# Optimization experiments

Measured on AMD Instinct MI355X. Metric: run time of the kernel, lower is better.

Reference implementation:

```python
import jax, jax.numpy as jnp
import numpy as np

LMDA = 1.0
SMOOTH = 1e-05

# 13 directional offsets (dz, dy, dx) matching the original slice pairs 1..13
OFFSETS = [
    (1, 0, 0), (0, 1, 0), (0, 0, 1),
    (1, 1, 0), (1, -1, 0),
    (0, 1, 1), (0, 1, -1),
    (1, 0, -1), (1, 0, 1),
    (1, -1, -1), (1, 1, -1),
    (-1, -1, -1), (-1, 1, -1),
]


def _shifted_diff(x, off):
    """x[..., pos-shift] - x[..., neg-shift] for offset off over last 3 dims."""
    sl_pos = tuple(slice(1, None) if o == 1 else (slice(None, -1) if o == -1 else slice(None)) for o in off)
    sl_neg = tuple(slice(None, -1) if o == 1 else (slice(1, None) if o == -1 else slice(None)) for o in off)
    return x[(Ellipsis,) + sl_pos] - x[(Ellipsis,) + sl_neg]


def setup_inputs() -> dict:
    key = jax.random.key(0)
    k1, k2 = jax.random.split(key)
    shape = (4, 1, 128, 192, 192)
    eps = 1e-6
    inp = jax.random.uniform(k1, shape, dtype=jnp.float32, minval=eps, maxval=1.0 - eps)
    tgt = jax.random.uniform(k2, shape, dtype=jnp.float32, minval=0.0, maxval=1.0)
    return {"input": inp, "target": tgt}


def reference(input, target):
    # region term: BCE with mean reduction
    bce = -jnp.mean(target * jnp.log(input) + (1.0 - target) * jnp.log(1.0 - input))

    # boundary term: 13 directional diff-product ratios
    acc = jnp.float32(0.0)
    for off in OFFSETS:
        di = _shifted_diff(input, off)
        dt = _shifted_diff(target, off)
        acc = acc + jnp.sum(di * dt) / (jnp.sum(dt * dt) + SMOOTH)
    boundary = 1.0 - acc / 13.0

    return LMDA * bce + boundary
```

## Files before the change

### kernel.cpp

```cpp
#include <hip/hip_runtime.h>
#include <math.h>

#define DX 192
#define DY 192
#define DZ 128
#define DB 4
#define DXY (DX*DY)
#define NTOT (DB*DZ*DXY)
#define XV (DX/4)
#define NCOL (DB*DZ*XV)
#define SEG 12
#define NSEG (DY/SEG)


__device__ inline float wred(float v) {
    #pragma unroll
    for (int o = 32; o > 0; o >>= 1) v += __shfl_down(v, o, 64);
    return v;
}

__device__ inline float4 ld4(const float* p) { return *(const float4*)p; }

#define TN(k, A1, A0, D1, D0) do { float di_=(A1)-(A0); float dt_=(D1)-(D0); \
    sk[k] += di_*dt_; rk[k] += dt_*dt_; } while(0)
#define TM(k, A1, A0, D1, D0) do { float di_=(A1)-(A0); float dt_=(D1)-(D0); \
    float dm_=fx3*dt_; sk[k] += di_*dm_; rk[k] += dt_*dm_; } while(0)
#define BCEACC(A0, D0) do { bces += (D0)*__logf(A0) + (1.0f-(D0))*__logf(1.0f-(A0)); } while(0)


#define ELEM_FULL(a0,a1,a2,a3,a4,a5,a6,a7, d0,d1,d2,d3,d4,d5,d6,d7) do { \
    TN(0,a4,a0,d4,d0); TN(1,a2,a0,d2,d0); TN(2,a1,a0,d1,d0); TN(3,a6,a0,d6,d0); \
    TN(4,a4,a2,d4,d2); TN(5,a3,a0,d3,d0); TN(6,a2,a1,d2,d1); TN(7,a4,a1,d4,d1); \
    TN(8,a5,a0,d5,d0); TN(9,a4,a3,d4,d3); TN(10,a6,a1,d6,d1); TN(11,a7,a0,d7,d0); \
    TN(12,a5,a2,d5,d2); BCEACC(a0,d0); } while(0)

#define ELEM_FX(a0,a1,a2,a3,a4,a5,a6,a7, d0,d1,d2,d3,d4,d5,d6,d7) do { \
    TN(0,a4,a0,d4,d0); TN(1,a2,a0,d2,d0); TM(2,a1,a0,d1,d0); TN(3,a6,a0,d6,d0); \
    TN(4,a4,a2,d4,d2); TM(5,a3,a0,d3,d0); TM(6,a2,a1,d2,d1); TM(7,a4,a1,d4,d1); \
    TM(8,a5,a0,d5,d0); TM(9,a4,a3,d4,d3); TM(10,a6,a1,d6,d1); TM(11,a7,a0,d7,d0); \
    TM(12,a5,a2,d5,d2); BCEACC(a0,d0); } while(0)

#define PEL_FULL(a0,a1,a4,a5, d0,d1,d4,d5) do { \
    TN(0,a4,a0,d4,d0); TN(2,a1,a0,d1,d0); TN(7,a4,a1,d4,d1); TN(8,a5,a0,d5,d0); \
    BCEACC(a0,d0); } while(0)
#define PEL_FX(a0,a1,a4,a5, d0,d1,d4,d5) do { \
    TN(0,a4,a0,d4,d0); TM(2,a1,a0,d1,d0); TM(7,a4,a1,d4,d1); TM(8,a5,a0,d5,d0); \
    BCEACC(a0,d0); } while(0)

#define ZEL_FULL(a0,a1,a2,a3, d0,d1,d2,d3) do { \
    TN(1,a2,a0,d2,d0); TN(2,a1,a0,d1,d0); TN(5,a3,a0,d3,d0); TN(6,a2,a1,d2,d1); \
    BCEACC(a0,d0); } while(0)
#define ZEL_FX(a0,a1,a2,a3, d0,d1,d2,d3) do { \
    TN(1,a2,a0,d2,d0); TM(2,a1,a0,d1,d0); TM(5,a3,a0,d3,d0); TM(6,a2,a1,d2,d1); \
    BCEACC(a0,d0); } while(0)

#define ZPEL_FULL(a0,a1, d0,d1) do { TN(2,a1,a0,d1,d0); BCEACC(a0,d0); } while(0)
#define ZPEL_FX(a0,a1, d0,d1)   do { TM(2,a1,a0,d1,d0); BCEACC(a0,d0); } while(0)

#define ROW_FULL(Ai0,Ai1,Aie, At0,At1,Ate, Bi0,Bi1,Bie, Bt0,Bt1,Bte) do { \
    ELEM_FULL(Ai0.x,Ai0.y, Bi0.x,Bi0.y, Ai1.x,Ai1.y, Bi1.x,Bi1.y, \
              At0.x,At0.y, Bt0.x,Bt0.y, At1.x,At1.y, Bt1.x,Bt1.y); \
    ELEM_FULL(Ai0.y,Ai0.z, Bi0.y,Bi0.z, Ai1.y,Ai1.z, Bi1.y,Bi1.z, \
              At0.y,At0.z, Bt0.y,Bt0.z, At1.y,At1.z, Bt1.y,Bt1.z); \
    ELEM_FULL(Ai0.z,Ai0.w, Bi0.z,Bi0.w, Ai1.z,Ai1.w, Bi1.z,Bi1.w, \
              At0.z,At0.w, Bt0.z,Bt0.w, At1.z,At1.w, Bt1.z,Bt1.w); \
    ELEM_FX  (Ai0.w,Aie,   Bi0.w,Bie,   Ai1.w,Ai1##e_, Bi1.w,Bi1##e_, \
              At0.w,Ate,   Bt0.w,Bte,   At1.w,At1##e_, Bt1.w,Bt1##e_); \
    } while(0)

__global__ __launch_bounds__(256) void gc3d_main(const float* __restrict__ inp,
                                                 const float* __restrict__ tgt,
                                                 double* __restrict__ acc) {
    float sk[13] = {0,0,0,0,0,0,0,0,0,0,0,0,0};
    float rk[13] = {0,0,0,0,0,0,0,0,0,0,0,0,0};
    float bces = 0.f;

    int c   = blockIdx.x * 256 + threadIdx.x;
    int s   = blockIdx.y;
    int xv4 = c % XV;
    int zb  = c / XV;
    int z   = zb & (DZ - 1);
    int y0  = s * SEG;
    bool xlast = (xv4 == XV - 1);
    int   xe   = xlast ? 3 : 4;
    float fx3  = xlast ? 0.f : 1.f;
    bool lastseg = (s == NSEG - 1);
    int  nfull   = SEG - (lastseg ? 1 : 0);

    int base = (zb * DY + y0) * DX + xv4 * 4;
    const float* ip = inp + base;
    const float* tp = tgt + base;

    if (z != DZ - 1) {
        float4 i0 = ld4(ip),        i1 = ld4(ip + DXY);
        float4 t0 = ld4(tp),        t1 = ld4(tp + DXY);
        float  i0e = ip[xe],        i1e = ip[DXY + xe];
        float  t0e = tp[xe],        t1e = tp[DXY + xe];
        float4 j0 = ld4(ip + DX),   j1 = ld4(ip + DX + DXY);
        float4 u0 = ld4(tp + DX),   u1 = ld4(tp + DX + DXY);
        float  j0e = ip[DX + xe],   j1e = ip[DX + DXY + xe];
        float  u0e = tp[DX + xe],   u1e = tp[DX + DXY + xe];

        #pragma unroll 2
        for (int it = 0; it < nfull - 1; ++it) {
            const float* ipk = ip + 2 * DX;
            const float* tpk = tp + 2 * DX;
            float4 k0 = ld4(ipk),       k1 = ld4(ipk + DXY);
            float4 w0 = ld4(tpk),       w1 = ld4(tpk + DXY);
            float  k0e = ipk[xe],       k1e = ipk[DXY + xe];
            float  w0e = tpk[xe],       w1e = tpk[DXY + xe];

            ELEM_FULL(i0.x,i0.y, j0.x,j0.y, i1.x,i1.y, j1.x,j1.y,
                      t0.x,t0.y, u0.x,u0.y, t1.x,t1.y, u1.x,u1.y);
            ELEM_FULL(i0.y,i0.z, j0.y,j0.z, i1.y,i1.z, j1.y,j1.z,
                      t0.y,t0.z, u0.y,u0.z, t1.y,t1.z, u1.y,u1.z);
            ELEM_FULL(i0.z,i0.w, j0.z,j0.w, i1.z,i1.w, j1.z,j1.w,
                      t0.z,t0.w, u0.z,u0.w, t1.z,t1.w, u1.z,u1.w);
            ELEM_FX  (i0.w,i0e,  j0.w,j0e,  i1.w,i1e,  j1.w,j1e,
                      t0.w,t0e,  u0.w,u0e,  t1.w,t1e,  u1.w,u1e);

            i0 = j0; i1 = j1; t0 = u0; t1 = u1;
            i0e = j0e; i1e = j1e; t0e = u0e; t1e = u1e;
            j0 = k0; j1 = k1; u0 = w0; u1 = w1;
            j0e = k0e; j1e = k1e; u0e = w0e; u1e = w1e;
            ip += DX; tp += DX;
        }
        ELEM_FULL(i0.x,i0.y, j0.x,j0.y, i1.x,i1.y, j1.x,j1.y,
                  t0.x,t0.y, u0.x,u0.y, t1.x,t1.y, u1.x,u1.y);
        ELEM_FULL(i0.y,i0.z, j0.y,j0.z, i1.y,i1.z, j1.y,j1.z,
                  t0.y,t0.z, u0.y,u0.z, t1.y,t1.z, u1.y,u1.z);
        ELEM_FULL(i0.z,i0.w, j0.z,j0.w, i1.z,i1.w, j1.z,j1.w,
                  t0.z,t0.w, u0.z,u0.w, t1.z,t1.w, u1.z,u1.w);
        ELEM_FX  (i0.w,i0e,  j0.w,j0e,  i1.w,i1e,  j1.w,j1e,
                  t0.w,t0e,  u0.w,u0e,  t1.w,t1e,  u1.w,u1e);

        if (lastseg) {
            PEL_FULL(j0.x,j0.y, j1.x,j1.y, u0.x,u0.y, u1.x,u1.y);
            PEL_FULL(j0.y,j0.z, j1.y,j1.z, u0.y,u0.z, u1.y,u1.z);
            PEL_FULL(j0.z,j0.w, j1.z,j1.w, u0.z,u0.w, u1.z,u1.w);
            PEL_FX  (j0.w,j0e,  j1.w,j1e,  u0.w,u0e,  u1.w,u1e);
        }
    } else {
        float4 i0 = ld4(ip);
        float4 t0 = ld4(tp);
        float  i0e = ip[xe];
        float  t0e = tp[xe];
        float4 j0 = ld4(ip + DX);
        float4 u0 = ld4(tp + DX);
        float  j0e = ip[DX + xe];
        float  u0e = tp[DX + xe];

        #pragma unroll 2
        for (int it = 0; it < nfull - 1; ++it) {
            const float* ipk = ip + 2 * DX;
            const float* tpk = tp + 2 * DX;
            float4 k0 = ld4(ipk);
            float4 w0 = ld4(tpk);
            float  k0e = ipk[xe];
            float  w0e = tpk[xe];

            ZEL_FULL(i0.x,i0.y, j0.x,j0.y, t0.x,t0.y, u0.x,u0.y);
            ZEL_FULL(i0.y,i0.z, j0.y,j0.z, t0.y,t0.z, u0.y,u0.z);
            ZEL_FULL(i0.z,i0.w, j0.z,j0.w, t0.z,t0.w, u0.z,u0.w);
            ZEL_FX  (i0.w,i0e,  j0.w,j0e,  t0.w,t0e,  u0.w,u0e);

            i0 = j0; t0 = u0; i0e = j0e; t0e = u0e;
            j0 = k0; u0 = w0; j0e = k0e; u0e = w0e;
            ip += DX; tp += DX;
        }
        ZEL_FULL(i0.x,i0.y, j0.x,j0.y, t0.x,t0.y, u0.x,u0.y);
        ZEL_FULL(i0.y,i0.z, j0.y,j0.z, t0.y,t0.z, u0.y,u0.z);
        ZEL_FULL(i0.z,i0.w, j0.z,j0.w, t0.z,t0.w, u0.z,u0.w);
        ZEL_FX  (i0.w,i0e,  j0.w,j0e,  t0.w,t0e,  u0.w,u0e);

        if (lastseg) {
            ZPEL_FULL(j0.x,j0.y, u0.x,u0.y);
            ZPEL_FULL(j0.y,j0.z, u0.y,u0.z);
            ZPEL_FULL(j0.z,j0.w, u0.z,u0.w);
            ZPEL_FX  (j0.w,j0e,  u0.w,u0e);
        }
    }

    float vals[27];
    #pragma unroll
    for (int q = 0; q < 13; q++) { vals[q] = sk[q]; vals[13 + q] = rk[q]; }
    vals[26] = bces;
    #pragma unroll
    for (int q = 0; q < 27; q++) vals[q] = wred(vals[q]);

    __shared__ float red[4][27];
    int lane = threadIdx.x & 63;
    int wave = threadIdx.x >> 6;
    if (lane == 0) {
        #pragma unroll
        for (int q = 0; q < 27; q++) red[wave][q] = vals[q];
    }
    __syncthreads();
    if (threadIdx.x < 27) {
        float t = red[0][threadIdx.x] + red[1][threadIdx.x]
                + red[2][threadIdx.x] + red[3][threadIdx.x];
        atomicAdd(&acc[threadIdx.x], (double)t);
    }
}

__global__ void gc3d_final(const double* __restrict__ acc, float* __restrict__ out) {
    if (threadIdx.x == 0 && blockIdx.x == 0) {
        double s = 0.0;
        #pragma unroll
        for (int k = 0; k < 13; k++) s += acc[k] / (acc[13 + k] + 1e-5);
        double bce = -acc[26] / (double)NTOT;
        out[0] = (float)(bce + 1.0 - s / 13.0);
    }
}

extern "C" void kernel_launch(void* const* d_in, const int* in_sizes, int n_in,
                              void* d_out, int out_size, void* d_ws, size_t ws_size,
                              hipStream_t stream) {
    const float* inp = (const float*)d_in[0];
    const float* tgt = (const float*)d_in[1];
    double* acc = (double*)d_ws;

    hipMemsetAsync(d_ws, 0, 27 * sizeof(double), stream);
    dim3 grid(NCOL / 256, NSEG);
    gc3d_main<<<grid, 256, 0, stream>>>(inp, tgt, acc);
    gc3d_final<<<1, 64, 0, stream>>>(acc, (float*)d_out);
}
```

Baseline: 214.5 us.

## Fully unroll row loop with deeper prefetch, smaller segments, occupancy bound

Shrinks the y-segment per thread from 12 to 8 rows, giving more blocks. The main (non-last-z) path becomes a fully unrolled sequence that loads up to three rows ahead before computing each row pair, which keeps more loads in flight. It also adds a min-blocks-per-CU launch bound of 3 to cap register use. The cost is more redundant halo-row loads per output row and more register pressure from the named row sets, which the launch bound may answer with spills.

```diff
diff --git a/kernel.cpp b/kernel.cpp
--- a/kernel.cpp
+++ b/kernel.cpp
@@ -9,7 +9,7 @@
 #define NTOT (DB*DZ*DXY)
 #define XV (DX/4)
 #define NCOL (DB*DZ*XV)
-#define SEG 12
+#define SEG 8
 #define NSEG (DY/SEG)
 
 
@@ -57,20 +57,36 @@
 #define ZPEL_FULL(a0,a1, d0,d1) do { TN(2,a1,a0,d1,d0); BCEACC(a0,d0); } while(0)
 #define ZPEL_FX(a0,a1, d0,d1)   do { TM(2,a1,a0,d1,d0); BCEACC(a0,d0); } while(0)
 
-#define ROW_FULL(Ai0,Ai1,Aie, At0,At1,Ate, Bi0,Bi1,Bie, Bt0,Bt1,Bte) do { \
-    ELEM_FULL(Ai0.x,Ai0.y, Bi0.x,Bi0.y, Ai1.x,Ai1.y, Bi1.x,Bi1.y, \
-              At0.x,At0.y, Bt0.x,Bt0.y, At1.x,At1.y, Bt1.x,Bt1.y); \
-    ELEM_FULL(Ai0.y,Ai0.z, Bi0.y,Bi0.z, Ai1.y,Ai1.z, Bi1.y,Bi1.z, \
-              At0.y,At0.z, Bt0.y,Bt0.z, At1.y,At1.z, Bt1.y,Bt1.z); \
-    ELEM_FULL(Ai0.z,Ai0.w, Bi0.z,Bi0.w, Ai1.z,Ai1.w, Bi1.z,Bi1.w, \
-              At0.z,At0.w, Bt0.z,Bt0.w, At1.z,At1.w, Bt1.z,Bt1.w); \
-    ELEM_FX  (Ai0.w,Aie,   Bi0.w,Bie,   Ai1.w,Ai1##e_, Bi1.w,Bi1##e_, \
-              At0.w,Ate,   Bt0.w,Bte,   At1.w,At1##e_, Bt1.w,Bt1##e_); \
+#define DECLSET(n) float4 i0_##n, i1_##n, t0_##n, t1_##n; \
+                   float  ie_##n, iz_##n, te_##n, tz_##n;
+
+#define LOADSET(n) do { \
+    i0_##n = ld4(ip  + n*DX); i1_##n = ld4(ipz + n*DX); \
+    t0_##n = ld4(tp  + n*DX); t1_##n = ld4(tpz + n*DX); \
+    ie_##n = ipe[n*DX]; iz_##n = ipze[n*DX]; \
+    te_##n = tpe[n*DX]; tz_##n = tpze[n*DX]; } while(0)
+
+#define COMP(a,b) do { \
+    ELEM_FULL(i0_##a.x,i0_##a.y, i0_##b.x,i0_##b.y, i1_##a.x,i1_##a.y, i1_##b.x,i1_##b.y, \
+              t0_##a.x,t0_##a.y, t0_##b.x,t0_##b.y, t1_##a.x,t1_##a.y, t1_##b.x,t1_##b.y); \
+    ELEM_FULL(i0_##a.y,i0_##a.z, i0_##b.y,i0_##b.z, i1_##a.y,i1_##a.z, i1_##b.y,i1_##b.z, \
+              t0_##a.y,t0_##a.z, t0_##b.y,t0_##b.z, t1_##a.y,t1_##a.z, t1_##b.y,t1_##b.z); \
+    ELEM_FULL(i0_##a.z,i0_##a.w, i0_##b.z,i0_##b.w, i1_##a.z,i1_##a.w, i1_##b.z,i1_##b.w, \
+              t0_##a.z,t0_##a.w, t0_##b.z,t0_##b.w, t1_##a.z,t1_##a.w, t1_##b.z,t1_##b.w); \
+    ELEM_FX  (i0_##a.w,ie_##a,  i0_##b.w,ie_##b,  i1_##a.w,iz_##a,  i1_##b.w,iz_##b, \
+              t0_##a.w,te_##a,  t0_##b.w,te_##b,  t1_##a.w,tz_##a,  t1_##b.w,tz_##b); \
     } while(0)
 
-__global__ __launch_bounds__(256) void gc3d_main(const float* __restrict__ inp,
-                                                 const float* __restrict__ tgt,
-                                                 double* __restrict__ acc) {
+#define PEEL(n) do { \
+    PEL_FULL(i0_##n.x,i0_##n.y, i1_##n.x,i1_##n.y, t0_##n.x,t0_##n.y, t1_##n.x,t1_##n.y); \
+    PEL_FULL(i0_##n.y,i0_##n.z, i1_##n.y,i1_##n.z, t0_##n.y,t0_##n.z, t1_##n.y,t1_##n.z); \
+    PEL_FULL(i0_##n.z,i0_##n.w, i1_##n.z,i1_##n.w, t0_##n.z,t0_##n.w, t1_##n.z,t1_##n.w); \
+    PEL_FX  (i0_##n.w,ie_##n,  i1_##n.w,iz_##n,  t0_##n.w,te_##n,  t1_##n.w,tz_##n); \
+    } while(0)
+
+__global__ __launch_bounds__(256, 3) void gc3d_main(const float* __restrict__ inp,
+                                                    const float* __restrict__ tgt,
+                                                    double* __restrict__ acc) {
     float sk[13] = {0,0,0,0,0,0,0,0,0,0,0,0,0};
     float rk[13] = {0,0,0,0,0,0,0,0,0,0,0,0,0};
     float bces = 0.f;
@@ -85,62 +101,45 @@
     int   xe   = xlast ? 3 : 4;
     float fx3  = xlast ? 0.f : 1.f;
     bool lastseg = (s == NSEG - 1);
-    int  nfull   = SEG - (lastseg ? 1 : 0);
 
     int base = (zb * DY + y0) * DX + xv4 * 4;
     const float* ip = inp + base;
     const float* tp = tgt + base;
 
     if (z != DZ - 1) {
-        float4 i0 = ld4(ip),        i1 = ld4(ip + DXY);
-        float4 t0 = ld4(tp),        t1 = ld4(tp + DXY);
-        float  i0e = ip[xe],        i1e = ip[DXY + xe];
-        float  t0e = tp[xe],        t1e = tp[DXY + xe];
-        float4 j0 = ld4(ip + DX),   j1 = ld4(ip + DX + DXY);
-        float4 u0 = ld4(tp + DX),   u1 = ld4(tp + DX + DXY);
-        float  j0e = ip[DX + xe],   j1e = ip[DX + DXY + xe];
-        float  u0e = tp[DX + xe],   u1e = tp[DX + DXY + xe];
-
-        #pragma unroll 2
-        for (int it = 0; it < nfull - 1; ++it) {
-            const float* ipk = ip + 2 * DX;
-            const float* tpk = tp + 2 * DX;
-            float4 k0 = ld4(ipk),       k1 = ld4(ipk + DXY);
-            float4 w0 = ld4(tpk),       w1 = ld4(tpk + DXY);
-            float  k0e = ipk[xe],       k1e = ipk[DXY + xe];
-            float  w0e = tpk[xe],       w1e = tpk[DXY + xe];
-
-            ELEM_FULL(i0.x,i0.y, j0.x,j0.y, i1.x,i1.y, j1.x,j1.y,
-                      t0.x,t0.y, u0.x,u0.y, t1.x,t1.y, u1.x,u1.y);
-            ELEM_FULL(i0.y,i0.z, j0.y,j0.z, i1.y,i1.z, j1.y,j1.z,
-                      t0.y,t0.z, u0.y,u0.z, t1.y,t1.z, u1.y,u1.z);
-            ELEM_FULL(i0.z,i0.w, j0.z,j0.w, i1.z,i1.w, j1.z,j1.w,
-                      t0.z,t0.w, u0.z,u0.w, t1.z,t1.w, u1.z,u1.w);
-            ELEM_FX  (i0.w,i0e,  j0.w,j0e,  i1.w,i1e,  j1.w,j1e,
-                      t0.w,t0e,  u0.w,u0e,  t1.w,t1e,  u1.w,u1e);
-
-            i0 = j0; i1 = j1; t0 = u0; t1 = u1;
-            i0e = j0e; i1e = j1e; t0e = u0e; t1e = u1e;
-            j0 = k0; j1 = k1; u0 = w0; u1 = w1;
-            j0e = k0e; j1e = k1e; u0e = w0e; u1e = w1e;
-            ip += DX; tp += DX;
-        }
-        ELEM_FULL(i0.x,i0.y, j0.x,j0.y, i1.x,i1.y, j1.x,j1.y,
-                  t0.x,t0.y, u0.x,u0.y, t1.x,t1.y, u1.x,u1.y);
-        ELEM_FULL(i0.y,i0.z, j0.y,j0.z, i1.y,i1.z, j1.y,j1.z,
-                  t0.y,t0.z, u0.y,u0.z, t1.y,t1.z, u1.y,u1.z);
-        ELEM_FULL(i0.z,i0.w, j0.z,j0.w, i1.z,i1.w, j1.z,j1.w,
-                  t0.z,t0.w, u0.z,u0.w, t1.z,t1.w, u1.z,u1.w);
-        ELEM_FX  (i0.w,i0e,  j0.w,j0e,  i1.w,i1e,  j1.w,j1e,
-                  t0.w,t0e,  u0.w,u0e,  t1.w,t1e,  u1.w,u1e);
-
-        if (lastseg) {
-            PEL_FULL(j0.x,j0.y, j1.x,j1.y, u0.x,u0.y, u1.x,u1.y);
-            PEL_FULL(j0.y,j0.z, j1.y,j1.z, u0.y,u0.z, u1.y,u1.z);
-            PEL_FULL(j0.z,j0.w, j1.z,j1.w, u0.z,u0.w, u1.z,u1.w);
-            PEL_FX  (j0.w,j0e,  j1.w,j1e,  u0.w,u0e,  u1.w,u1e);
+        const float* ipz  = ip + DXY;
+        const float* tpz  = tp + DXY;
+        const float* ipe  = ip  + xe;
+        const float* ipze = ipz + xe;
+        const float* tpe  = tp  + xe;
+        const float* tpze = tpz + xe;
+
+        DECLSET(0) DECLSET(1) DECLSET(2) DECLSET(3) DECLSET(4)
+        DECLSET(5) DECLSET(6) DECLSET(7) DECLSET(8)
+
+        if (!lastseg) {
+            LOADSET(0); LOADSET(1); LOADSET(2);
+            LOADSET(3); COMP(0,1);
+            LOADSET(4); COMP(1,2);
+            LOADSET(5); COMP(2,3);
+            LOADSET(6); COMP(3,4);
+            LOADSET(7); COMP(4,5);
+            LOADSET(8); COMP(5,6);
+            COMP(6,7);
+            COMP(7,8);
+        } else {
+            LOADSET(0); LOADSET(1); LOADSET(2);
+            LOADSET(3); COMP(0,1);
+            LOADSET(4); COMP(1,2);
+            LOADSET(5); COMP(2,3);
+            LOADSET(6); COMP(3,4);
+            LOADSET(7); COMP(4,5);
+            COMP(5,6);
+            COMP(6,7);
+            PEEL(7);
         }
     } else {
+        int nfull = SEG - (lastseg ? 1 : 0);
         float4 i0 = ld4(ip);
         float4 t0 = ld4(tp);
         float  i0e = ip[xe];
```

Result: slower. 323.0 us (+50.6%).
